# Kernel optimization log

Hardware: AMD Instinct MI355X
Metric: run time of the kernel (lower is better)

## Reference

```python
import jax, jax.numpy as jnp
import numpy as np

N, E, IN_FT, OUT_FT = 20000, 4096, 128, 128


def setup_inputs() -> dict:
    key = jax.random.key(0)
    kx, kh, kw = jax.random.split(key, 3)
    X = jax.random.normal(kx, (N, IN_FT), dtype=jnp.float32)
    H = jax.random.randint(kh, (N, E), 0, 2, dtype=jnp.int32)
    weight = jax.random.normal(kw, (IN_FT, OUT_FT), dtype=jnp.float32) * (1.0 / np.sqrt(IN_FT))
    bias = jnp.zeros((OUT_FT,), dtype=jnp.float32)
    return {"X": X, "H": H, "weight": weight, "bias": bias}


def reference(X, H, weight, bias):
    # Dv^{-1/2} H De^{-1} H^T Dv^{-1/2} X W + b, with diag matrices fused as
    # row/column scalings (same math as the torch.diag @ chain, no NxN temporaries).
    Hf = H.astype(jnp.float32)
    v_deg = jnp.sum(Hf, axis=1)            # [N]
    e_deg = jnp.sum(Hf, axis=0)            # [E]
    v_deg = jnp.where(v_deg > 0, v_deg, 1.0)
    e_deg = jnp.where(e_deg > 0, e_deg, 1.0)
    dv_inv_sqrt = 1.0 / jnp.sqrt(v_deg)    # diag(Dv^-1/2)
    de_inv = 1.0 / e_deg                   # diag(De^-1)
    Y = dv_inv_sqrt[:, None] * X
    T = Hf.T @ Y                           # H^T (...)        [E, in]
    T = de_inv[:, None] * T                # De^-1 (...)
    Z = Hf @ T                             # H (...)          [N, in]
    Z = dv_inv_sqrt[:, None] * Z           # Dv^-1/2 (...)
    out = Z @ weight + bias                # [N, out]
    return out
```

## Files before the change

kernel.cpp:

```cpp
#include <hip/hip_runtime.h>

#define NV 20000
#define NE 4096
#define FT 128
#define NW_E 128
#define NW_V 625
#define NVP 20032

typedef __attribute__((ext_vector_type(8))) short short8v;
typedef __attribute__((ext_vector_type(4))) float float4v;

__device__ __forceinline__ unsigned short f2bf(float f) {
    unsigned u = __float_as_uint(f);
    u += 0x7FFFu + ((u >> 16) & 1u);
    return (unsigned short)(u >> 16);
}
__device__ __forceinline__ int lds_off(int r, int chunk) {
    return r * 128 + ((chunk ^ (r & 7)) << 4);
}
__device__ __forceinline__ uint4 lut_entry(int t) {
    uint4 e;
    e.x = ((t & 1) ? 0x3F80u : 0u) | ((t & 2) ? 0x3F800000u : 0u);
    e.y = ((t & 4) ? 0x3F80u : 0u) | ((t & 8) ? 0x3F800000u : 0u);
    e.z = ((t & 16) ? 0x3F80u : 0u) | ((t & 32) ? 0x3F800000u : 0u);
    e.w = ((t & 64) ? 0x3F80u : 0u) | ((t & 128) ? 0x3F800000u : 0u);
    return e;
}

__global__ __launch_bounds__(256) void k_packt(const int* __restrict__ H,
                                               unsigned* __restrict__ packed,
                                               unsigned* __restrict__ packedT,
                                               int* __restrict__ dvp) {
    __shared__ int cl[64];
    int b = blockIdx.x;
    int g = b >> 1, h = b & 1;
    int t = threadIdx.x, lane = t & 63;
    int w0 = h * 64 + (t >> 6) * 16;
    int n = g * 64 + lane;
    bool valid = n < NV;
    const uint4* base = reinterpret_cast<const uint4*>(H) + (size_t)n * (NE / 4);

    if (t < 64) cl[t] = 0;
    __syncthreads();

    int cnt = 0;
    int nw = g * 2 + (lane >> 5);
    for (int it = 0; it < 16; ++it) {
        int w = w0 + it;
        unsigned m = 0;
        if (valid) {
            const uint4* p = base + w * 8;
#pragma unroll
            for (int i = 0; i < 8; ++i) {
                uint4 v = p[i];
                m |= (v.x ? 1u : 0u) << (i * 4 + 0);
                m |= (v.y ? 1u : 0u) << (i * 4 + 1);
                m |= (v.z ? 1u : 0u) << (i * 4 + 2);
                m |= (v.w ? 1u : 0u) << (i * 4 + 3);
            }
            packed[(size_t)n * NW_E + w] = m;
        }
        cnt += __popc(m);
        unsigned my = 0;
#pragma unroll
        for (int j = 0; j < 32; ++j) {
            unsigned long long bm = __ballot(((m >> j) & 1u) != 0);
            unsigned part = (lane < 32) ? (unsigned)bm : (unsigned)(bm >> 32);
            if ((lane & 31) == j) my = part;
        }
        int e = w * 32 + (lane & 31);
        if (nw < NW_V) packedT[(size_t)e * NW_V + nw] = my;
    }
    atomicAdd(&cl[lane], cnt);
    __syncthreads();
    if (t < 64) dvp[h * NVP + g * 64 + t] = cl[t];
}

__global__ __launch_bounds__(256) void k_mid(const unsigned* __restrict__ packedT,
                                             const int* __restrict__ dvp,
                                             const float* __restrict__ X,
                                             float* __restrict__ de,
                                             float* __restrict__ dv,
                                             unsigned short* __restrict__ Ybf) {
    int b = blockIdx.x, t = threadIdx.x;
    if (b < 1024) {
        int lane = t & 63, w = t >> 6;
        int e = b * 4 + w;
        const unsigned* row = packedT + (size_t)e * NW_V;
        int c = 0;
        for (int i = lane; i < NW_V; i += 64) c += __popc(row[i]);
        for (int o = 32; o > 0; o >>= 1) c += __shfl_down(c, o, 64);
        if (lane == 0) de[e] = c > 0 ? 1.0f / (float)c : 1.0f;
    } else if (b < 1024 + 79) {
        int i = (b - 1024) * 256 + t;
        if (i < NV) {
            int d = dvp[i] + dvp[NVP + i];
            dv[i] = d > 0 ? 1.0f / sqrtf((float)d) : 1.0f;
        }
    } else {
        int b2 = b - 1103;
        int f = t & 127;
        int nb = (b2 * 2 + (t >> 7)) * 8;
        unsigned short h[8];
#pragma unroll
        for (int i = 0; i < 8; ++i) {
            int n = nb + i;
            int d = dvp[n] + dvp[NVP + n];
            float s = d > 0 ? 1.0f / sqrtf((float)d) : 1.0f;
            h[i] = f2bf(X[(size_t)n * FT + f] * s);
        }
        uint4 u;
        u.x = (unsigned)h[0] | ((unsigned)h[1] << 16);
        u.y = (unsigned)h[2] | ((unsigned)h[3] << 16);
        u.z = (unsigned)h[4] | ((unsigned)h[5] << 16);
        u.w = (unsigned)h[6] | ((unsigned)h[7] << 16);
        *reinterpret_cast<uint4*>(Ybf + (size_t)f * NV + nb) = u;
    }
}

__global__ __launch_bounds__(256, 2) void k_mm1(const unsigned short* __restrict__ Ybf,
                                                const unsigned* __restrict__ packedT,
                                                float* __restrict__ P, int chunkK) {
    __shared__ __align__(16) unsigned char sA[128 * 128];
    __shared__ __align__(16) unsigned char sB[128 * 128];
    __shared__ __align__(16) uint4 slut[256];
    int t = threadIdx.x;
    slut[t] = lut_entry(t & 255);

    int et = blockIdx.x & 31, kp = blockIdx.x >> 5;
    int e0 = et * 128;
    int kbeg = kp * chunkK;
    int iters = chunkK >> 6;

    float4v acc[4][4];
#pragma unroll
    for (int i = 0; i < 4; ++i)
#pragma unroll
        for (int j = 0; j < 4; ++j)
#pragma unroll
            for (int r = 0; r < 4; ++r) acc[i][j][r] = 0.0f;

    int fA = t & 127;
    int chbA = (t >> 7) * 4;
    const unsigned short* arow = Ybf + (size_t)fA * NV;
    int eB = t & 127;
    int hB = t >> 7;
    const unsigned* brow = packedT + (size_t)(e0 + eB) * NW_V;

    int wave = t >> 6, lane = t & 63;
    int wm0 = (wave & 1) * 64, wc0 = (wave >> 1) * 64;
    int r0 = lane & 15, q = lane >> 4;
    __syncthreads();

    for (int it = 0; it < iters; ++it) {
        int k0 = kbeg + it * 64;
#pragma unroll
        for (int c = 0; c < 4; ++c) {
            int ch = chbA + c;
            int n = k0 + ch * 8;
            uint4 v = {0, 0, 0, 0};
            if (n < NV) v = *reinterpret_cast<const uint4*>(arow + n);
            *reinterpret_cast<uint4*>(sA + lds_off(fA, ch)) = v;
        }
        {
            int nw = (k0 >> 5) + hB;
            unsigned wv = (nw < NW_V) ? brow[nw] : 0u;
#pragma unroll
            for (int c = 0; c < 4; ++c) {
                uint4 u = slut[(wv >> (c * 8)) & 0xFF];
                *reinterpret_cast<uint4*>(sB + lds_off(eB, hB * 4 + c)) = u;
            }
        }
        __syncthreads();
#pragma unroll
        for (int ks = 0; ks < 2; ++ks) {
            short8v a[4], bb[4];
#pragma unroll
            for (int mi = 0; mi < 4; ++mi)
                a[mi] = *reinterpret_cast<const short8v*>(sA + lds_off(wm0 + mi * 16 + r0, ks * 4 + q));
#pragma unroll
            for (int ci = 0; ci < 4; ++ci)
                bb[ci] = *reinterpret_cast<const short8v*>(sB + lds_off(wc0 + ci * 16 + r0, ks * 4 + q));
#pragma unroll
            for (int mi = 0; mi < 4; ++mi)
#pragma unroll
                for (int ci = 0; ci < 4; ++ci)
                    acc[mi][ci] = __builtin_amdgcn_mfma_f32_16x16x32_bf16(a[mi], bb[ci], acc[mi][ci], 0, 0, 0);
        }
        __syncthreads();
    }
    float* Pp = P + (size_t)kp * (128 * 4096);
#pragma unroll
    for (int mi = 0; mi < 4; ++mi)
#pragma unroll
        for (int ci = 0; ci < 4; ++ci) {
            int f = wm0 + mi * 16 + q * 4;
            int e = e0 + wc0 + ci * 16 + r0;
#pragma unroll
            for (int r = 0; r < 4; ++r)
                Pp[(size_t)(f + r) * 4096 + e] = acc[mi][ci][r];
        }
}

__global__ __launch_bounds__(256) void k_reduce(const float4v* __restrict__ P,
                                                float4v* __restrict__ Tt, int S) {
    int i = blockIdx.x * 256 + threadIdx.x;
    float4v a = P[i];
    for (int p = 1; p < S; ++p) a += P[(size_t)p * 131072 + i];
    Tt[i] = a;
}

__global__ __launch_bounds__(256) void k_ut(const float* __restrict__ Tt,
                                            const float* __restrict__ W,
                                            const float* __restrict__ de,
                                            unsigned short* __restrict__ Ubf) {
    int t = threadIdx.x;
    int e = blockIdx.x * 64 + (t & 63);
    int g0 = blockIdx.y * 16 + (t >> 6) * 4;
    float a0 = 0, a1 = 0, a2 = 0, a3 = 0;
    for (int f = 0; f < 128; ++f) {
        float tv = Tt[(size_t)f * 4096 + e];
        float4 wv = *reinterpret_cast<const float4*>(W + f * 128 + g0);
        a0 += tv * wv.x; a1 += tv * wv.y; a2 += tv * wv.z; a3 += tv * wv.w;
    }
    float d = de[e];
    Ubf[(size_t)(g0 + 0) * 4096 + e] = f2bf(a0 * d);
    Ubf[(size_t)(g0 + 1) * 4096 + e] = f2bf(a1 * d);
    Ubf[(size_t)(g0 + 2) * 4096 + e] = f2bf(a2 * d);
    Ubf[(size_t)(g0 + 3) * 4096 + e] = f2bf(a3 * d);
}

__global__ __launch_bounds__(256, 4) void k_mm2(const unsigned* __restrict__ packed,
                                                const unsigned short* __restrict__ Ubf,
                                                const float* __restrict__ dv,
                                                const float* __restrict__ bias,
                                                float* __restrict__ out) {
    __shared__ __align__(16) unsigned char sA[128 * 128];
    __shared__ __align__(16) unsigned char sB[32 * 128];
    __shared__ __align__(16) uint4 slut[256];
    int t = threadIdx.x;
    slut[t] = lut_entry(t & 255);

    int mt = blockIdx.x >> 2, qg = blockIdx.x & 3;
    int n0 = mt * 128, g0 = qg * 32;

    float4v acc[4];
#pragma unroll
    for (int i = 0; i < 4; ++i)
#pragma unroll
        for (int r = 0; r < 4; ++r) acc[i][r] = 0.0f;

    int nA = t & 127, hA = t >> 7;
    int rB = t & 31, cB = t >> 5;
    const unsigned short* brow = Ubf + (size_t)(g0 + rB) * 4096;

    int wave = t >> 6, lane = t & 63;
    int wm0 = (wave & 1) * 64, wc0 = (wave >> 1) * 16;
    int r0 = lane & 15, q = lane >> 4;
    __syncthreads();

    for (int k0 = 0; k0 < 4096; k0 += 64) {
        {
            unsigned wv = (n0 + nA < NV) ? packed[(size_t)(n0 + nA) * NW_E + (k0 >> 5) + hA] : 0u;
#pragma unroll
            for (int c = 0; c < 4; ++c) {
                uint4 u = slut[(wv >> (c * 8)) & 0xFF];
                *reinterpret_cast<uint4*>(sA + lds_off(nA, hA * 4 + c)) = u;
            }
        }
        {
            uint4 v = *reinterpret_cast<const uint4*>(brow + k0 + cB * 8);
            *reinterpret_cast<uint4*>(sB + lds_off(rB, cB)) = v;
        }
        __syncthreads();
#pragma unroll
        for (int ks = 0; ks < 2; ++ks) {
            short8v a[4], bb;
#pragma unroll
            for (int mi = 0; mi < 4; ++mi)
                a[mi] = *reinterpret_cast<const short8v*>(sA + lds_off(wm0 + mi * 16 + r0, ks * 4 + q));
            bb = *reinterpret_cast<const short8v*>(sB + lds_off(wc0 + r0, ks * 4 + q));
#pragma unroll
            for (int mi = 0; mi < 4; ++mi)
                acc[mi] = __builtin_amdgcn_mfma_f32_16x16x32_bf16(a[mi], bb, acc[mi], 0, 0, 0);
        }
        __syncthreads();
    }
    {
        int g = g0 + wc0 + r0;
        float bg = bias[g];
#pragma unroll
        for (int mi = 0; mi < 4; ++mi) {
#pragma unroll
            for (int r = 0; r < 4; ++r) {
                int n = n0 + wm0 + mi * 16 + q * 4 + r;
                if (n < NV) out[(size_t)n * 128 + g] = dv[n] * acc[mi][r] + bg;
            }
        }
    }
}

extern "C" void kernel_launch(void* const* d_in, const int* in_sizes, int n_in,
                              void* d_out, int out_size, void* d_ws, size_t ws_size,
                              hipStream_t stream) {
    const float* X    = (const float*)d_in[0];
    const int*   H    = (const int*)d_in[1];
    const float* W    = (const float*)d_in[2];
    const float* bias = (const float*)d_in[3];
    float* out = (float*)d_out;

    char* ws = (char*)d_ws;
    size_t off = 0;
    auto alloc = [&](size_t sz) { char* p = ws + off; off += (sz + 255) & ~(size_t)255; return p; };
    unsigned*       packed  = (unsigned*)alloc((size_t)NV * NW_E * 4);
    unsigned*       packedT = (unsigned*)alloc((size_t)NE * NW_V * 4);
    unsigned short* Ybf     = (unsigned short*)alloc((size_t)FT * NV * 2);
    float*          Tt      = (float*)alloc((size_t)FT * NE * 4);
    unsigned short* Ubf     = (unsigned short*)alloc((size_t)FT * NE * 2);
    float*          dv      = (float*)alloc((size_t)NV * 4);
    float*          de      = (float*)alloc((size_t)NE * 4);
    int*            dvp     = (int*)alloc((size_t)2 * NVP * 4);
    size_t fixed = off;

    long long avail = (long long)ws_size - (long long)fixed;
    int S = (int)(avail / (128LL * 4096 * 4));
    if (S > 16) S = 16;
    if (S < 1) S = 1;
    float* P1 = (float*)(ws + fixed);
    int chunkK = ((NV + S * 64 - 1) / (S * 64)) * 64;

    k_packt <<<626, 256, 0, stream>>>(H, packed, packedT, dvp);
    k_mid   <<<2353, 256, 0, stream>>>(packedT, dvp, X, de, dv, Ybf);
    k_mm1   <<<32 * S, 256, 0, stream>>>(Ybf, packedT, P1, chunkK);
    k_reduce<<<512, 256, 0, stream>>>((const float4v*)P1, (float4v*)Tt, S);
    k_ut    <<<dim3(64, 8), 256, 0, stream>>>(Tt, W, de, Ubf);
    k_mm2   <<<628, 256, 0, stream>>>(packed, Ubf, dv, bias, out);
}
```

Before: 636.1 us.

## Fuse all stages into one cooperative persistent kernel with grid syncs

Replaces six separate kernel launches with a single cooperative kernel of 512 blocks that runs packing, degree/scale computation, the split-K first GEMM, the reduction, the weight projection and the second GEMM as phases separated by grid-wide syncs. This removes per-launch overhead and the gaps between dependent kernels. The first GEMM is also retiled to 128x64 tiles with a fixed split-K of 8, chosen to match the 512-block grid. In exchange, each phase is capped at 512 resident blocks, the second GEMM loses its 4-blocks-per-CU occupancy hint, and grid syncs add their own cost.

```diff
diff --git a/kernel.cpp b/kernel.cpp
--- a/kernel.cpp
+++ b/kernel.cpp
@@ -1,4 +1,7 @@
 #include <hip/hip_runtime.h>
+#include <hip/hip_cooperative_groups.h>
+
+namespace cg = cooperative_groups;
 
 #define NV 20000
 #define NE 4096
@@ -6,6 +9,8 @@
 #define NW_E 128
 #define NW_V 625
 #define NVP 20032
+#define SPLITK 8
+#define CHUNKK 2560
 
 typedef __attribute__((ext_vector_type(8))) short short8v;
 typedef __attribute__((ext_vector_type(4))) float float4v;
@@ -27,274 +32,266 @@
     return e;
 }
 
-__global__ __launch_bounds__(256) void k_packt(const int* __restrict__ H,
-                                               unsigned* __restrict__ packed,
-                                               unsigned* __restrict__ packedT,
-                                               int* __restrict__ dvp) {
-    __shared__ int cl[64];
-    int b = blockIdx.x;
-    int g = b >> 1, h = b & 1;
-    int t = threadIdx.x, lane = t & 63;
-    int w0 = h * 64 + (t >> 6) * 16;
-    int n = g * 64 + lane;
-    bool valid = n < NV;
-    const uint4* base = reinterpret_cast<const uint4*>(H) + (size_t)n * (NE / 4);
-
-    if (t < 64) cl[t] = 0;
-    __syncthreads();
-
-    int cnt = 0;
-    int nw = g * 2 + (lane >> 5);
-    for (int it = 0; it < 16; ++it) {
-        int w = w0 + it;
-        unsigned m = 0;
-        if (valid) {
-            const uint4* p = base + w * 8;
+__global__ __launch_bounds__(256, 2) void k_mega(
+    const int* __restrict__ H, const float* __restrict__ X,
+    const float* __restrict__ W, const float* __restrict__ bias,
+    float* __restrict__ out,
+    unsigned* __restrict__ packed, unsigned* __restrict__ packedT,
+    int* __restrict__ dvp, unsigned short* __restrict__ Ybf,
+    float* __restrict__ P, float* __restrict__ Tt,
+    unsigned short* __restrict__ Ubf, float* __restrict__ dv,
+    float* __restrict__ de) {
+
+    __shared__ __align__(16) unsigned char sA[16384];
+    __shared__ __align__(16) unsigned char sB[8192];
+    __shared__ __align__(16) uint4 slut[256];
+
+    cg::grid_group grid = cg::this_grid();
+    int t = threadIdx.x;
+    int wave = t >> 6, lane = t & 63;
+    int r0 = lane & 15, q = lane >> 4;
+
+    slut[t] = lut_entry(t);
+
+    {
+        int* cl = (int*)sA;
+        for (int v = blockIdx.x; v < 626; v += 512) {
+            int g = v >> 1, h = v & 1;
+            int w0 = h * 64 + wave * 16;
+            int n = g * 64 + lane;
+            bool valid = n < NV;
+            const uint4* base = reinterpret_cast<const uint4*>(H) + (size_t)n * (NE / 4);
+
+            if (t < 64) cl[t] = 0;
+            __syncthreads();
+
+            int cnt = 0;
+            int nw = g * 2 + (lane >> 5);
+            for (int it = 0; it < 16; ++it) {
+                int w = w0 + it;
+                unsigned m = 0;
+                if (valid) {
+                    const uint4* p = base + w * 8;
+#pragma unroll
+                    for (int i = 0; i < 8; ++i) {
+                        uint4 vv = p[i];
+                        m |= (vv.x ? 1u : 0u) << (i * 4 + 0);
+                        m |= (vv.y ? 1u : 0u) << (i * 4 + 1);
+                        m |= (vv.z ? 1u : 0u) << (i * 4 + 2);
+                        m |= (vv.w ? 1u : 0u) << (i * 4 + 3);
+                    }
+                    packed[(size_t)n * NW_E + w] = m;
+                }
+                cnt += __popc(m);
+                unsigned my = 0;
+#pragma unroll
+                for (int j = 0; j < 32; ++j) {
+                    unsigned long long bm = __ballot(((m >> j) & 1u) != 0);
+                    unsigned part = (lane < 32) ? (unsigned)bm : (unsigned)(bm >> 32);
+                    if ((lane & 31) == j) my = part;
+                }
+                int e = w * 32 + (lane & 31);
+                if (nw < NW_V) packedT[(size_t)e * NW_V + nw] = my;
+            }
+            atomicAdd(&cl[lane], cnt);
+            __syncthreads();
+            if (t < 64) dvp[h * NVP + g * 64 + t] = cl[t];
+            __syncthreads();
+        }
+    }
+    grid.sync();
+
+    for (int v = blockIdx.x; v < 2353; v += 512) {
+        if (v < 1024) {
+            int e = v * 4 + wave;
+            const unsigned* row = packedT + (size_t)e * NW_V;
+            int c = 0;
+            for (int i = lane; i < NW_V; i += 64) c += __popc(row[i]);
+            for (int o = 32; o > 0; o >>= 1) c += __shfl_down(c, o, 64);
+            if (lane == 0) de[e] = c > 0 ? 1.0f / (float)c : 1.0f;
+        } else if (v < 1024 + 79) {
+            int i = (v - 1024) * 256 + t;
+            if (i < NV) {
+                int d = dvp[i] + dvp[NVP + i];
+                dv[i] = d > 0 ? 1.0f / sqrtf((float)d) : 1.0f;
+            }
+        } else {
+            int b2 = v - 1103;
+            int f = t & 127;
+            int nb = (b2 * 2 + (t >> 7)) * 8;
+            unsigned short h[8];
 #pragma unroll
             for (int i = 0; i < 8; ++i) {
-                uint4 v = p[i];
-                m |= (v.x ? 1u : 0u) << (i * 4 + 0);
-                m |= (v.y ? 1u : 0u) << (i * 4 + 1);
-                m |= (v.z ? 1u : 0u) << (i * 4 + 2);
-                m |= (v.w ? 1u : 0u) << (i * 4 + 3);
-            }
-            packed[(size_t)n * NW_E + w] = m;
-        }
-        cnt += __popc(m);
-        unsigned my = 0;
-#pragma unroll
-        for (int j = 0; j < 32; ++j) {
-            unsigned long long bm = __ballot(((m >> j) & 1u) != 0);
-            unsigned part = (lane < 32) ? (unsigned)bm : (unsigned)(bm >> 32);
-            if ((lane & 31) == j) my = part;
-        }
-        int e = w * 32 + (lane & 31);
-        if (nw < NW_V) packedT[(size_t)e * NW_V + nw] = my;
-    }
-    atomicAdd(&cl[lane], cnt);
-    __syncthreads();
-    if (t < 64) dvp[h * NVP + g * 64 + t] = cl[t];
-}
-
-__global__ __launch_bounds__(256) void k_mid(const unsigned* __restrict__ packedT,
-                                             const int* __restrict__ dvp,
-                                             const float* __restrict__ X,
-                                             float* __restrict__ de,
-                                             float* __restrict__ dv,
-                                             unsigned short* __restrict__ Ybf) {
-    int b = blockIdx.x, t = threadIdx.x;
-    if (b < 1024) {
-        int lane = t & 63, w = t >> 6;
-        int e = b * 4 + w;
-        const unsigned* row = packedT + (size_t)e * NW_V;
-        int c = 0;
-        for (int i = lane; i < NW_V; i += 64) c += __popc(row[i]);
-        for (int o = 32; o > 0; o >>= 1) c += __shfl_down(c, o, 64);
-        if (lane == 0) de[e] = c > 0 ? 1.0f / (float)c : 1.0f;
-    } else if (b < 1024 + 79) {
-        int i = (b - 1024) * 256 + t;
-        if (i < NV) {
-            int d = dvp[i] + dvp[NVP + i];
-            dv[i] = d > 0 ? 1.0f / sqrtf((float)d) : 1.0f;
-        }
-    } else {
-        int b2 = b - 1103;
-        int f = t & 127;
-        int nb = (b2 * 2 + (t >> 7)) * 8;
-        unsigned short h[8];
-#pragma unroll
-        for (int i = 0; i < 8; ++i) {
-            int n = nb + i;
-            int d = dvp[n] + dvp[NVP + n];
-            float s = d > 0 ? 1.0f / sqrtf((float)d) : 1.0f;
-            h[i] = f2bf(X[(size_t)n * FT + f] * s);
-        }
-        uint4 u;
-        u.x = (unsigned)h[0] | ((unsigned)h[1] << 16);
-        u.y = (unsigned)h[2] | ((unsigned)h[3] << 16);
-        u.z = (unsigned)h[4] | ((unsigned)h[5] << 16);
-        u.w = (unsigned)h[6] | ((unsigned)h[7] << 16);
-        *reinterpret_cast<uint4*>(Ybf + (size_t)f * NV + nb) = u;
-    }
-}
-
-__global__ __launch_bounds__(256, 2) void k_mm1(const unsigned short* __restrict__ Ybf,
-                                                const unsigned* __restrict__ packedT,
-                                                float* __restrict__ P, int chunkK) {
-    __shared__ __align__(16) unsigned char sA[128 * 128];
-    __shared__ __align__(16) unsigned char sB[128 * 128];
-    __shared__ __align__(16) uint4 slut[256];
-    int t = threadIdx.x;
-    slut[t] = lut_entry(t & 255);
-
-    int et = blockIdx.x & 31, kp = blockIdx.x >> 5;
-    int e0 = et * 128;
-    int kbeg = kp * chunkK;
-    int iters = chunkK >> 6;
-
-    float4v acc[4][4];
-#pragma unroll
-    for (int i = 0; i < 4; ++i)
-#pragma unroll
-        for (int j = 0; j < 4; ++j)
-#pragma unroll
-            for (int r = 0; r < 4; ++r) acc[i][j][r] = 0.0f;
-
-    int fA = t & 127;
-    int chbA = (t >> 7) * 4;
-    const unsigned short* arow = Ybf + (size_t)fA * NV;
-    int eB = t & 127;
-    int hB = t >> 7;
-    const unsigned* brow = packedT + (size_t)(e0 + eB) * NW_V;
-
-    int wave = t >> 6, lane = t & 63;
-    int wm0 = (wave & 1) * 64, wc0 = (wave >> 1) * 64;
-    int r0 = lane & 15, q = lane >> 4;
-    __syncthreads();
-
-    for (int it = 0; it < iters; ++it) {
-        int k0 = kbeg + it * 64;
-#pragma unroll
-        for (int c = 0; c < 4; ++c) {
-            int ch = chbA + c;
-            int n = k0 + ch * 8;
-            uint4 v = {0, 0, 0, 0};
-            if (n < NV) v = *reinterpret_cast<const uint4*>(arow + n);
-            *reinterpret_cast<uint4*>(sA + lds_off(fA, ch)) = v;
+                int n = nb + i;
+                int d = dvp[n] + dvp[NVP + n];
+                float s = d > 0 ? 1.0f / sqrtf((float)d) : 1.0f;
+                h[i] = f2bf(X[(size_t)n * FT + f] * s);
+            }
+            uint4 u;
+            u.x = (unsigned)h[0] | ((unsigned)h[1] << 16);
+            u.y = (unsigned)h[2] | ((unsigned)h[3] << 16);
+            u.z = (unsigned)h[4] | ((unsigned)h[5] << 16);
+            u.w = (unsigned)h[6] | ((unsigned)h[7] << 16);
+            *reinterpret_cast<uint4*>(Ybf + (size_t)f * NV + nb) = u;
+        }
+    }
+    grid.sync();
+
+    {
+        int et = blockIdx.x & 63, kp = blockIdx.x >> 6;
+        int e0 = et * 64;
+        int kbeg = kp * CHUNKK;
+
+        float4v acc[4][2];
+#pragma unroll
+        for (int i = 0; i < 4; ++i)
+#pragma unroll
+            for (int j = 0; j < 2; ++j)
+#pragma unroll
+                for (int r = 0; r < 4; ++r) acc[i][j][r] = 0.0f;
+
+        int fA = t & 127;
+        int chbA = (t >> 7) * 4;
+        const unsigned short* arow = Ybf + (size_t)fA * NV;
+        int rB = t & 63, wsel = (t >> 6) & 1, bsel = t >> 7;
+        const unsigned* brow = packedT + (size_t)(e0 + rB) * NW_V;
+
+        int wm0 = (wave & 1) * 64, wc0 = (wave >> 1) * 32;
+
+        for (int it = 0; it < CHUNKK / 64; ++it) {
+            int k0 = kbeg + it * 64;
+#pragma unroll
+            for (int c = 0; c < 4; ++c) {
+                int ch = chbA + c;
+                int n = k0 + ch * 8;
+                uint4 v = {0, 0, 0, 0};
+                if (n < NV) v = *reinterpret_cast<const uint4*>(arow + n);
+                *reinterpret_cast<uint4*>(sA + lds_off(fA, ch)) = v;
+            }
+            {
+                int nw = (k0 >> 5) + wsel;
+                unsigned wv = (nw < NW_V) ? brow[nw] : 0u;
+#pragma unroll
+                for (int c = 0; c < 2; ++c) {
+                    int byte = bsel * 2 + c;
+                    uint4 u = slut[(wv >> (byte * 8)) & 0xFF];
+                    *reinterpret_cast<uint4*>(sB + lds_off(rB, wsel * 4 + byte)) = u;
+                }
+            }
+            __syncthreads();
+#pragma unroll
+            for (int ks = 0; ks < 2; ++ks) {
+                short8v a[4], bb[2];
+#pragma unroll
+                for (int mi = 0; mi < 4; ++mi)
+                    a[mi] = *reinterpret_cast<const short8v*>(sA + lds_off(wm0 + mi * 16 + r0, ks * 4 + q));
+#pragma unroll
+                for (int ci = 0; ci < 2; ++ci)
+                    bb[ci] = *reinterpret_cast<const short8v*>(sB + lds_off(wc0 + ci * 16 + r0, ks * 4 + q));
+#pragma unroll
+                for (int mi = 0; mi < 4; ++mi)
+#pragma unroll
+                    for (int ci = 0; ci < 2; ++ci)
+                        acc[mi][ci] = __builtin_amdgcn_mfma_f32_16x16x32_bf16(a[mi], bb[ci], acc[mi][ci], 0, 0, 0);
+            }
+            __syncthreads();
+        }
+        float* Pp = P + (size_t)kp * (128 * 4096);
+#pragma unroll
+        for (int mi = 0; mi < 4; ++mi)
+#pragma unroll
+            for (int ci = 0; ci < 2; ++ci) {
+                int f = wm0 + mi * 16 + q * 4;
+                int e = e0 + wc0 + ci * 16 + r0;
+#pragma unroll
+                for (int r = 0; r < 4; ++r)
+                    Pp[(size_t)(f + r) * 4096 + e] = acc[mi][ci][r];
+            }
+    }
+    grid.sync();
+
+    {
+        int i = blockIdx.x * 256 + t;
+        const float4v* Pv = (const float4v*)P;
+        float4v a = Pv[i];
+#pragma unroll
+        for (int p = 1; p < SPLITK; ++p) a += Pv[(size_t)p * 131072 + i];
+        ((float4v*)Tt)[i] = a;
+    }
+    grid.sync();
+
+    {
+        int bx = blockIdx.x & 63, by = blockIdx.x >> 6;
+        int e = bx * 64 + (t & 63);
+        int g0 = by * 16 + (t >> 6) * 4;
+        float a0 = 0, a1 = 0, a2 = 0, a3 = 0;
+        for (int f = 0; f < 128; ++f) {
+            float tv = Tt[(size_t)f * 4096 + e];
+            float4 wv = *reinterpret_cast<const float4*>(W + f * 128 + g0);
+            a0 += tv * wv.x; a1 += tv * wv.y; a2 += tv * wv.z; a3 += tv * wv.w;
+        }
+        float d = de[e];
+        Ubf[(size_t)(g0 + 0) * 4096 + e] = f2bf(a0 * d);
+        Ubf[(size_t)(g0 + 1) * 4096 + e] = f2bf(a1 * d);
+        Ubf[(size_t)(g0 + 2) * 4096 + e] = f2bf(a2 * d);
+        Ubf[(size_t)(g0 + 3) * 4096 + e] = f2bf(a3 * d);
+    }
+    grid.sync();
+
+    for (int v = blockIdx.x; v < 628; v += 512) {
+        int mt = v >> 2, qg = v & 3;
+        int n0 = mt * 128, g0 = qg * 32;
+
+        float4v acc[4];
+#pragma unroll
+        for (int i = 0; i < 4; ++i)
+#pragma unroll
+            for (int r = 0; r < 4; ++r) acc[i][r] = 0.0f;
+
+        int nA = t & 127, hA = t >> 7;
+        int rB = t & 31, cB = t >> 5;
+        const unsigned short* brow = Ubf + (size_t)(g0 + rB) * 4096;
+
+        int wm0 = (wave & 1) * 64, wc0 = (wave >> 1) * 16;
+        __syncthreads();
+
+        for (int k0 = 0; k0 < 4096; k0 += 64) {
+            {
+                unsigned wv = (n0 + nA < NV) ? packed[(size_t)(n0 + nA) * NW_E + (k0 >> 5) + hA] : 0u;
+#pragma unroll
+                for (int c = 0; c < 4; ++c) {
+                    uint4 u = slut[(wv >> (c * 8)) & 0xFF];
+                    *reinterpret_cast<uint4*>(sA + lds_off(nA, hA * 4 + c)) = u;
+                }
+            }
+            {
+                uint4 v2 = *reinterpret_cast<const uint4*>(brow + k0 + cB * 8);
+                *reinterpret_cast<uint4*>(sB + lds_off(rB, cB)) = v2;
+            }
+            __syncthreads();
+#pragma unroll
+            for (int ks = 0; ks < 2; ++ks) {
+                short8v a[4], bb;
+#pragma unroll
+                for (int mi = 0; mi < 4; ++mi)
+                    a[mi] = *reinterpret_cast<const short8v*>(sA + lds_off(wm0 + mi * 16 + r0, ks * 4 + q));
+                bb = *reinterpret_cast<const short8v*>(sB + lds_off(wc0 + r0, ks * 4 + q));
+#pragma unroll
+                for (int mi = 0; mi < 4; ++mi)
+                    acc[mi] = __builtin_amdgcn_mfma_f32_16x16x32_bf16(a[mi], bb, acc[mi], 0, 0, 0);
+            }
+            __syncthreads();
         }
         {
-            int nw = (k0 >> 5) + hB;
-            unsigned wv = (nw < NW_V) ? brow[nw] : 0u;
-#pragma unroll
-            for (int c = 0; c < 4; ++c) {
-                uint4 u = slut[(wv >> (c * 8)) & 0xFF];
-                *reinterpret_cast<uint4*>(sB + lds_off(eB, hB * 4 + c)) = u;
-            }
-        }
-        __syncthreads();
-#pragma unroll
-        for (int ks = 0; ks < 2; ++ks) {
-            short8v a[4], bb[4];
-#pragma unroll
-            for (int mi = 0; mi < 4; ++mi)
-                a[mi] = *reinterpret_cast<const short8v*>(sA + lds_off(wm0 + mi * 16 + r0, ks * 4 + q));
-#pragma unroll
-            for (int ci = 0; ci < 4; ++ci)
-                bb[ci] = *reinterpret_cast<const short8v*>(sB + lds_off(wc0 + ci * 16 + r0, ks * 4 + q));
-#pragma unroll
-            for (int mi = 0; mi < 4; ++mi)
-#pragma unroll
-                for (int ci = 0; ci < 4; ++ci)
-                    acc[mi][ci] = __builtin_amdgcn_mfma_f32_16x16x32_bf16(a[mi], bb[ci], acc[mi][ci], 0, 0, 0);
-        }
-        __syncthreads();
-    }
-    float* Pp = P + (size_t)kp * (128 * 4096);
-#pragma unroll
-    for (int mi = 0; mi < 4; ++mi)
-#pragma unroll
-        for (int ci = 0; ci < 4; ++ci) {
-            int f = wm0 + mi * 16 + q * 4;
-            int e = e0 + wc0 + ci * 16 + r0;
-#pragma unroll
-            for (int r = 0; r < 4; ++r)
-                Pp[(size_t)(f + r) * 4096 + e] = acc[mi][ci][r];
-        }
-}
-
-__global__ __launch_bounds__(256) void k_reduce(const float4v* __restrict__ P,
-                                                float4v* __restrict__ Tt, int S) {
-    int i = blockIdx.x * 256 + threadIdx.x;
-    float4v a = P[i];
-    for (int p = 1; p < S; ++p) a += P[(size_t)p * 131072 + i];
-    Tt[i] = a;
-}
-
-__global__ __launch_bounds__(256) void k_ut(const float* __restrict__ Tt,
-                                            const float* __restrict__ W,
-                                            const float* __restrict__ de,
-                                            unsigned short* __restrict__ Ubf) {
-    int t = threadIdx.x;
-    int e = blockIdx.x * 64 + (t & 63);
-    int g0 = blockIdx.y * 16 + (t >> 6) * 4;
-    float a0 = 0, a1 = 0, a2 = 0, a3 = 0;
-    for (int f = 0; f < 128; ++f) {
-        float tv = Tt[(size_t)f * 4096 + e];
-        float4 wv = *reinterpret_cast<const float4*>(W + f * 128 + g0);
-        a0 += tv * wv.x; a1 += tv * wv.y; a2 += tv * wv.z; a3 += tv * wv.w;
-    }
-    float d = de[e];
-    Ubf[(size_t)(g0 + 0) * 4096 + e] = f2bf(a0 * d);
-    Ubf[(size_t)(g0 + 1) * 4096 + e] = f2bf(a1 * d);
-    Ubf[(size_t)(g0 + 2) * 4096 + e] = f2bf(a2 * d);
-    Ubf[(size_t)(g0 + 3) * 4096 + e] = f2bf(a3 * d);
-}
-
-__global__ __launch_bounds__(256, 4) void k_mm2(const unsigned* __restrict__ packed,
-                                                const unsigned short* __restrict__ Ubf,
-                                                const float* __restrict__ dv,
-                                                const float* __restrict__ bias,
-                                                float* __restrict__ out) {
-    __shared__ __align__(16) unsigned char sA[128 * 128];
-    __shared__ __align__(16) unsigned char sB[32 * 128];
-    __shared__ __align__(16) uint4 slut[256];
-    int t = threadIdx.x;
-    slut[t] = lut_entry(t & 255);
-
-    int mt = blockIdx.x >> 2, qg = blockIdx.x & 3;
-    int n0 = mt * 128, g0 = qg * 32;
-
-    float4v acc[4];
-#pragma unroll
-    for (int i = 0; i < 4; ++i)
-#pragma unroll
-        for (int r = 0; r < 4; ++r) acc[i][r] = 0.0f;
-
-    int nA = t & 127, hA = t >> 7;
-    int rB = t & 31, cB = t >> 5;
-    const unsigned short* brow = Ubf + (size_t)(g0 + rB) * 4096;
-
-    int wave = t >> 6, lane = t & 63;
-    int wm0 = (wave & 1) * 64, wc0 = (wave >> 1) * 16;
-    int r0 = lane & 15, q = lane >> 4;
-    __syncthreads();
-
-    for (int k0 = 0; k0 < 4096; k0 += 64) {
-        {
-            unsigned wv = (n0 + nA < NV) ? packed[(size_t)(n0 + nA) * NW_E + (k0 >> 5) + hA] : 0u;
-#pragma unroll
-            for (int c = 0; c < 4; ++c) {
-                uint4 u = slut[(wv >> (c * 8)) & 0xFF];
-                *reinterpret_cast<uint4*>(sA + lds_off(nA, hA * 4 + c)) = u;
-            }
-        }
-        {
-            uint4 v = *reinterpret_cast<const uint4*>(brow + k0 + cB * 8);
-            *reinterpret_cast<uint4*>(sB + lds_off(rB, cB)) = v;
-        }
-        __syncthreads();
-#pragma unroll
-        for (int ks = 0; ks < 2; ++ks) {
-            short8v a[4], bb;
-#pragma unroll
-            for (int mi = 0; mi < 4; ++mi)
-                a[mi] = *reinterpret_cast<const short8v*>(sA + lds_off(wm0 + mi * 16 + r0, ks * 4 + q));
-            bb = *reinterpret_cast<const short8v*>(sB + lds_off(wc0 + r0, ks * 4 + q));
-#pragma unroll
-            for (int mi = 0; mi < 4; ++mi)
-                acc[mi] = __builtin_amdgcn_mfma_f32_16x16x32_bf16(a[mi], bb, acc[mi], 0, 0, 0);
-        }
-        __syncthreads();
-    }
-    {
-        int g = g0 + wc0 + r0;
-        float bg = bias[g];
-#pragma unroll
-        for (int mi = 0; mi < 4; ++mi) {
-#pragma unroll
-            for (int r = 0; r < 4; ++r) {
-                int n = n0 + wm0 + mi * 16 + q * 4 + r;
-                if (n < NV) out[(size_t)n * 128 + g] = dv[n] * acc[mi][r] + bg;
+            int g = g0 + wc0 + r0;
+            float bg = bias[g];
+#pragma unroll
+            for (int mi = 0; mi < 4; ++mi) {
+#pragma unroll
+                for (int r = 0; r < 4; ++r) {
+                    int n = n0 + wm0 + mi * 16 + q * 4 + r;
+                    if (n < NV) out[(size_t)n * 128 + g] = dv[n] * acc[mi][r] + bg;
+                }
             }
         }
     }
@@ -303,8 +300,8 @@
 extern "C" void kernel_launch(void* const* d_in, const int* in_sizes, int n_in,
                               void* d_out, int out_size, void* d_ws, size_t ws_size,
                               hipStream_t stream) {
+    const int*   H    = (const int*)d_in[1];
     const float* X    = (const float*)d_in[0];
-    const int*   H    = (const int*)d_in[1];
     const float* W    = (const float*)d_in[2];
     const float* bias = (const float*)d_in[3];
     float* out = (float*)d_out;
@@ -320,19 +317,11 @@
     float*          dv      = (float*)alloc((size_t)NV * 4);
     float*          de      = (float*)alloc((size_t)NE * 4);
     int*            dvp     = (int*)alloc((size_t)2 * NVP * 4);
-    size_t fixed = off;
-
-    long long avail = (long long)ws_size - (long long)fixed;
-    int S = (int)(avail / (128LL * 4096 * 4));
-    if (S > 16) S = 16;
-    if (S < 1) S = 1;
-    float* P1 = (float*)(ws + fixed);
-    int chunkK = ((NV + S * 64 - 1) / (S * 64)) * 64;
-
-    k_packt <<<626, 256, 0, stream>>>(H, packed, packedT, dvp);
-    k_mid   <<<2353, 256, 0, stream>>>(packedT, dvp, X, de, dv, Ybf);
-    k_mm1   <<<32 * S, 256, 0, stream>>>(Ybf, packedT, P1, chunkK);
-    k_reduce<<<512, 256, 0, stream>>>((const float4v*)P1, (float4v*)Tt, S);
-    k_ut    <<<dim3(64, 8), 256, 0, stream>>>(Tt, W, de, Ubf);
-    k_mm2   <<<628, 256, 0, stream>>>(packed, Ubf, dv, bias, out);
-}
+    float*          P1      = (float*)alloc((size_t)SPLITK * FT * NE * 4);
+
+    void* args[] = {(void*)&H, (void*)&X, (void*)&W, (void*)&bias, (void*)&out,
+                    (void*)&packed, (void*)&packedT, (void*)&dvp, (void*)&Ybf,
+                    (void*)&P1, (void*)&Tt, (void*)&Ubf, (void*)&dv, (void*)&de};
+    hipLaunchCooperativeKernel(reinterpret_cast<void*>(k_mega), dim3(512), dim3(256),
+                               args, 0, stream);
+}
```

After: 1.015 ms. 1.6x slower.

## Split packing into coalesced row pack and bit-transpose, tile operands into contiguous slabs

Applied to the files above, without the earlier changes.

The combined pack/transpose kernel becomes two kernels. One reads each H row contiguously with two waves per row, computes the vertex degree scale directly, and writes the bitmask. The other does the ballot bit-transpose into a padded packedT stride. The matmul operands (scaled X and the U matrix) are stored in per-K-chunk contiguous 64-wide slabs so the GEMM tile loads are fully coalesced, and the bitmask words are prefetched as uint4 one iteration ahead. The aim is to cut the strided, poorly coalesced reads of the 328MB H input and of the GEMM tiles, at the cost of an extra launch and an extra pass over the packed bitmask.

```diff
diff --git a/kernel.cpp b/kernel.cpp
--- a/kernel.cpp
+++ b/kernel.cpp
@@ -5,7 +5,8 @@
 #define FT 128
 #define NW_E 128
 #define NW_V 625
-#define NVP 20032
+#define PT_STRIDE 632
+#define NKC 313
 
 typedef __attribute__((ext_vector_type(8))) short short8v;
 typedef __attribute__((ext_vector_type(4))) float float4v;
@@ -27,110 +28,106 @@
     return e;
 }
 
-__global__ __launch_bounds__(256) void k_packt(const int* __restrict__ H,
-                                               unsigned* __restrict__ packed,
-                                               unsigned* __restrict__ packedT,
-                                               int* __restrict__ dvp) {
-    __shared__ int cl[64];
-    int b = blockIdx.x;
-    int g = b >> 1, h = b & 1;
-    int t = threadIdx.x, lane = t & 63;
-    int w0 = h * 64 + (t >> 6) * 16;
-    int n = g * 64 + lane;
-    bool valid = n < NV;
-    const uint4* base = reinterpret_cast<const uint4*>(H) + (size_t)n * (NE / 4);
-
-    if (t < 64) cl[t] = 0;
+__global__ __launch_bounds__(256) void k_pack(const int* __restrict__ H,
+                                              unsigned* __restrict__ packed,
+                                              float* __restrict__ dv) {
+    __shared__ int cl[4];
+    int t = threadIdx.x, wave = t >> 6, lane = t & 63;
+    int row = blockIdx.x * 2 + (wave >> 1);
+    int half = wave & 1;
+    const uint4* base = reinterpret_cast<const uint4*>(H) + (size_t)row * 1024 + half * 512 + lane * 8;
+    unsigned m = 0;
+#pragma unroll
+    for (int i = 0; i < 8; ++i) {
+        uint4 v = base[i];
+        m |= (v.x ? 1u : 0u) << (i * 4 + 0);
+        m |= (v.y ? 1u : 0u) << (i * 4 + 1);
+        m |= (v.z ? 1u : 0u) << (i * 4 + 2);
+        m |= (v.w ? 1u : 0u) << (i * 4 + 3);
+    }
+    packed[(size_t)row * NW_E + half * 64 + lane] = m;
+    int c = __popc(m);
+    for (int o = 32; o > 0; o >>= 1) c += __shfl_down(c, o, 64);
+    if (lane == 0) cl[wave] = c;
     __syncthreads();
-
-    int cnt = 0;
-    int nw = g * 2 + (lane >> 5);
-    for (int it = 0; it < 16; ++it) {
-        int w = w0 + it;
-        unsigned m = 0;
-        if (valid) {
-            const uint4* p = base + w * 8;
-#pragma unroll
-            for (int i = 0; i < 8; ++i) {
-                uint4 v = p[i];
-                m |= (v.x ? 1u : 0u) << (i * 4 + 0);
-                m |= (v.y ? 1u : 0u) << (i * 4 + 1);
-                m |= (v.z ? 1u : 0u) << (i * 4 + 2);
-                m |= (v.w ? 1u : 0u) << (i * 4 + 3);
-            }
-            packed[(size_t)n * NW_E + w] = m;
-        }
-        cnt += __popc(m);
-        unsigned my = 0;
-#pragma unroll
-        for (int j = 0; j < 32; ++j) {
-            unsigned long long bm = __ballot(((m >> j) & 1u) != 0);
-            unsigned part = (lane < 32) ? (unsigned)bm : (unsigned)(bm >> 32);
-            if ((lane & 31) == j) my = part;
-        }
-        int e = w * 32 + (lane & 31);
-        if (nw < NW_V) packedT[(size_t)e * NW_V + nw] = my;
-    }
-    atomicAdd(&cl[lane], cnt);
-    __syncthreads();
-    if (t < 64) dvp[h * NVP + g * 64 + t] = cl[t];
+    if (t < 2) {
+        int d = cl[t * 2] + cl[t * 2 + 1];
+        dv[blockIdx.x * 2 + t] = d > 0 ? 1.0f / sqrtf((float)d) : 1.0f;
+    }
+}
+
+__global__ __launch_bounds__(256) void k_btrans(const unsigned* __restrict__ packed,
+                                                unsigned* __restrict__ packedT) {
+    int lane = threadIdx.x & 63;
+    int w = threadIdx.x >> 6;
+    int ew = blockIdx.y * 4 + w;
+    int n = blockIdx.x * 64 + lane;
+    unsigned wv = (n < NV) ? packed[(size_t)n * NW_E + ew] : 0u;
+    unsigned my = 0;
+#pragma unroll
+    for (int j = 0; j < 32; ++j) {
+        unsigned long long m = __ballot(((wv >> j) & 1u) != 0);
+        unsigned part = (lane < 32) ? (unsigned)m : (unsigned)(m >> 32);
+        if ((lane & 31) == j) my = part;
+    }
+    int nw = blockIdx.x * 2 + (lane >> 5);
+    int e = ew * 32 + (lane & 31);
+    if (nw <= 625) packedT[(size_t)e * PT_STRIDE + nw] = my;
 }
 
 __global__ __launch_bounds__(256) void k_mid(const unsigned* __restrict__ packedT,
-                                             const int* __restrict__ dvp,
                                              const float* __restrict__ X,
+                                             const float* __restrict__ dv,
                                              float* __restrict__ de,
-                                             float* __restrict__ dv,
-                                             unsigned short* __restrict__ Ybf) {
+                                             unsigned short* __restrict__ At) {
     int b = blockIdx.x, t = threadIdx.x;
+    int wave = t >> 6, lane = t & 63;
     if (b < 1024) {
-        int lane = t & 63, w = t >> 6;
-        int e = b * 4 + w;
-        const unsigned* row = packedT + (size_t)e * NW_V;
+        int e = b * 4 + wave;
+        const unsigned* row = packedT + (size_t)e * PT_STRIDE;
         int c = 0;
         for (int i = lane; i < NW_V; i += 64) c += __popc(row[i]);
         for (int o = 32; o > 0; o >>= 1) c += __shfl_down(c, o, 64);
         if (lane == 0) de[e] = c > 0 ? 1.0f / (float)c : 1.0f;
-    } else if (b < 1024 + 79) {
-        int i = (b - 1024) * 256 + t;
-        if (i < NV) {
-            int d = dvp[i] + dvp[NVP + i];
-            dv[i] = d > 0 ? 1.0f / sqrtf((float)d) : 1.0f;
-        }
-    } else {
-        int b2 = b - 1103;
+    } else if (b < 2274) {
+        int b2 = b - 1024;
         int f = t & 127;
         int nb = (b2 * 2 + (t >> 7)) * 8;
         unsigned short h[8];
 #pragma unroll
         for (int i = 0; i < 8; ++i) {
             int n = nb + i;
-            int d = dvp[n] + dvp[NVP + n];
-            float s = d > 0 ? 1.0f / sqrtf((float)d) : 1.0f;
-            h[i] = f2bf(X[(size_t)n * FT + f] * s);
+            h[i] = f2bf(X[(size_t)n * FT + f] * dv[n]);
         }
         uint4 u;
         u.x = (unsigned)h[0] | ((unsigned)h[1] << 16);
         u.y = (unsigned)h[2] | ((unsigned)h[3] << 16);
         u.z = (unsigned)h[4] | ((unsigned)h[5] << 16);
         u.w = (unsigned)h[6] | ((unsigned)h[7] << 16);
-        *reinterpret_cast<uint4*>(Ybf + (size_t)f * NV + nb) = u;
-    }
-}
-
-__global__ __launch_bounds__(256, 2) void k_mm1(const unsigned short* __restrict__ Ybf,
+        int kc = nb >> 6;
+        *reinterpret_cast<uint4*>(At + (size_t)kc * 8192 + f * 64 + (nb & 63)) = u;
+    } else {
+        int f = t & 127;
+        uint4 z = {0, 0, 0, 0};
+        *reinterpret_cast<uint4*>(At + (size_t)312 * 8192 + f * 64 + 32 + (t >> 7) * 8) = z;
+        *reinterpret_cast<uint4*>(At + (size_t)312 * 8192 + f * 64 + 48 + (t >> 7) * 8) = z;
+    }
+}
+
+__global__ __launch_bounds__(256, 2) void k_mm1(const unsigned short* __restrict__ At,
                                                 const unsigned* __restrict__ packedT,
                                                 float* __restrict__ P, int chunkK) {
-    __shared__ __align__(16) unsigned char sA[128 * 128];
-    __shared__ __align__(16) unsigned char sB[128 * 128];
+    __shared__ __align__(16) unsigned char sA[16384];
+    __shared__ __align__(16) unsigned char sB[16384];
     __shared__ __align__(16) uint4 slut[256];
     int t = threadIdx.x;
-    slut[t] = lut_entry(t & 255);
+    slut[t] = lut_entry(t);
 
     int et = blockIdx.x & 31, kp = blockIdx.x >> 5;
     int e0 = et * 128;
     int kbeg = kp * chunkK;
-    int iters = chunkK >> 6;
+    int kend = kbeg + chunkK; if (kend > NKC * 64) kend = NKC * 64;
+    int iters = (kend - kbeg) >> 6; if (iters < 0) iters = 0;
 
     float4v acc[4][4];
 #pragma unroll
@@ -139,37 +136,41 @@
         for (int j = 0; j < 4; ++j)
 #pragma unroll
             for (int r = 0; r < 4; ++r) acc[i][j][r] = 0.0f;
-
-    int fA = t & 127;
-    int chbA = (t >> 7) * 4;
-    const unsigned short* arow = Ybf + (size_t)fA * NV;
-    int eB = t & 127;
-    int hB = t >> 7;
-    const unsigned* brow = packedT + (size_t)(e0 + eB) * NW_V;
 
     int wave = t >> 6, lane = t & 63;
     int wm0 = (wave & 1) * 64, wc0 = (wave >> 1) * 64;
     int r0 = lane & 15, q = lane >> 4;
+
+    const unsigned* brow = packedT + (size_t)(e0 + (t & 127)) * PT_STRIDE + (kbeg >> 5);
+    uint4 bw, bw2;
+    if (t < 128) bw = *reinterpret_cast<const uint4*>(brow);
     __syncthreads();
 
     for (int it = 0; it < iters; ++it) {
-        int k0 = kbeg + it * 64;
+        int kc = (kbeg >> 6) + it;
+        const uint4* slab = reinterpret_cast<const uint4*>(At + (size_t)kc * 8192);
 #pragma unroll
         for (int c = 0; c < 4; ++c) {
-            int ch = chbA + c;
-            int n = k0 + ch * 8;
-            uint4 v = {0, 0, 0, 0};
-            if (n < NV) v = *reinterpret_cast<const uint4*>(arow + n);
-            *reinterpret_cast<uint4*>(sA + lds_off(fA, ch)) = v;
-        }
-        {
-            int nw = (k0 >> 5) + hB;
-            unsigned wv = (nw < NW_V) ? brow[nw] : 0u;
-#pragma unroll
-            for (int c = 0; c < 4; ++c) {
-                uint4 u = slut[(wv >> (c * 8)) & 0xFF];
-                *reinterpret_cast<uint4*>(sB + lds_off(eB, hB * 4 + c)) = u;
+            int idx = c * 256 + t;
+            uint4 v = slab[idx];
+            *reinterpret_cast<uint4*>(sA + lds_off(idx >> 3, idx & 7)) = v;
+        }
+        if (t < 128) {
+            unsigned w0, w1;
+            if (!(it & 1)) {
+                bw2 = *reinterpret_cast<const uint4*>(brow + 2 * it + 4);
+                w0 = bw.x; w1 = bw.y;
+            } else {
+                w0 = bw.z; w1 = bw.w;
             }
+            int rB = t;
+#pragma unroll
+            for (int c = 0; c < 4; ++c)
+                *reinterpret_cast<uint4*>(sB + lds_off(rB, c)) = slut[(w0 >> (c * 8)) & 0xFF];
+#pragma unroll
+            for (int c = 0; c < 4; ++c)
+                *reinterpret_cast<uint4*>(sB + lds_off(rB, 4 + c)) = slut[(w1 >> (c * 8)) & 0xFF];
+            if (it & 1) bw = bw2;
         }
         __syncthreads();
 #pragma unroll
@@ -213,9 +214,10 @@
 __global__ __launch_bounds__(256) void k_ut(const float* __restrict__ Tt,
                                             const float* __restrict__ W,
                                             const float* __restrict__ de,
-                                            unsigned short* __restrict__ Ubf) {
+                                            unsigned short* __restrict__ Ut) {
     int t = threadIdx.x;
-    int e = blockIdx.x * 64 + (t & 63);
+    int bx = blockIdx.x;
+    int e = bx * 64 + (t & 63);
     int g0 = blockIdx.y * 16 + (t >> 6) * 4;
     float a0 = 0, a1 = 0, a2 = 0, a3 = 0;
     for (int f = 0; f < 128; ++f) {
@@ -224,22 +226,23 @@
         a0 += tv * wv.x; a1 += tv * wv.y; a2 += tv * wv.z; a3 += tv * wv.w;
     }
     float d = de[e];
-    Ubf[(size_t)(g0 + 0) * 4096 + e] = f2bf(a0 * d);
-    Ubf[(size_t)(g0 + 1) * 4096 + e] = f2bf(a1 * d);
-    Ubf[(size_t)(g0 + 2) * 4096 + e] = f2bf(a2 * d);
-    Ubf[(size_t)(g0 + 3) * 4096 + e] = f2bf(a3 * d);
+    int j = t & 63;
+    Ut[(size_t)bx * 8192 + (g0 + 0) * 64 + j] = f2bf(a0 * d);
+    Ut[(size_t)bx * 8192 + (g0 + 1) * 64 + j] = f2bf(a1 * d);
+    Ut[(size_t)bx * 8192 + (g0 + 2) * 64 + j] = f2bf(a2 * d);
+    Ut[(size_t)bx * 8192 + (g0 + 3) * 64 + j] = f2bf(a3 * d);
 }
 
 __global__ __launch_bounds__(256, 4) void k_mm2(const unsigned* __restrict__ packed,
-                                                const unsigned short* __restrict__ Ubf,
+                                                const unsigned short* __restrict__ Ut,
                                                 const float* __restrict__ dv,
                                                 const float* __restrict__ bias,
                                                 float* __restrict__ out) {
-    __shared__ __align__(16) unsigned char sA[128 * 128];
-    __shared__ __align__(16) unsigned char sB[32 * 128];
+    __shared__ __align__(16) unsigned char sA[16384];
+    __shared__ __align__(16) unsigned char sB[4096];
     __shared__ __align__(16) uint4 slut[256];
     int t = threadIdx.x;
-    slut[t] = lut_entry(t & 255);
+    slut[t] = lut_entry(t);
 
     int mt = blockIdx.x >> 2, qg = blockIdx.x & 3;
     int n0 = mt * 128, g0 = qg * 32;
@@ -249,28 +252,43 @@
     for (int i = 0; i < 4; ++i)
 #pragma unroll
         for (int r = 0; r < 4; ++r) acc[i][r] = 0.0f;
-
-    int nA = t & 127, hA = t >> 7;
-    int rB = t & 31, cB = t >> 5;
-    const unsigned short* brow = Ubf + (size_t)(g0 + rB) * 4096;
 
     int wave = t >> 6, lane = t & 63;
     int wm0 = (wave & 1) * 64, wc0 = (wave >> 1) * 16;
     int r0 = lane & 15, q = lane >> 4;
+
+    const unsigned* arow = packed + (size_t)(n0 + (t & 127)) * NW_E;
+    const unsigned short* bbase = Ut + (size_t)qg * 2048;
+    int t2 = t - 128;
+    uint4 aw, aw2;
+    if (t < 128) aw = *reinterpret_cast<const uint4*>(arow);
     __syncthreads();
 
-    for (int k0 = 0; k0 < 4096; k0 += 64) {
-        {
-            unsigned wv = (n0 + nA < NV) ? packed[(size_t)(n0 + nA) * NW_E + (k0 >> 5) + hA] : 0u;
-#pragma unroll
-            for (int c = 0; c < 4; ++c) {
-                uint4 u = slut[(wv >> (c * 8)) & 0xFF];
-                *reinterpret_cast<uint4*>(sA + lds_off(nA, hA * 4 + c)) = u;
+    for (int it = 0; it < 64; ++it) {
+        if (t < 128) {
+            unsigned w0, w1;
+            if (!(it & 1)) {
+                aw2 = *reinterpret_cast<const uint4*>(arow + 2 * it + 4);
+                w0 = aw.x; w1 = aw.y;
+            } else {
+                w0 = aw.z; w1 = aw.w;
             }
-        }
-        {
-            uint4 v = *reinterpret_cast<const uint4*>(brow + k0 + cB * 8);
-            *reinterpret_cast<uint4*>(sB + lds_off(rB, cB)) = v;
+            int rA = t;
+#pragma unroll
+            for (int c = 0; c < 4; ++c)
+                *reinterpret_cast<uint4*>(sA + lds_off(rA, c)) = slut[(w0 >> (c * 8)) & 0xFF];
+#pragma unroll
+            for (int c = 0; c < 4; ++c)
+                *reinterpret_cast<uint4*>(sA + lds_off(rA, 4 + c)) = slut[(w1 >> (c * 8)) & 0xFF];
+            if (it & 1) aw = aw2;
+        } else {
+            const uint4* src = reinterpret_cast<const uint4*>(bbase + (size_t)it * 8192);
+#pragma unroll
+            for (int c = 0; c < 2; ++c) {
+                int idx = t2 * 2 + c;
+                uint4 v = src[idx];
+                *reinterpret_cast<uint4*>(sB + lds_off(idx >> 3, idx & 7)) = v;
+            }
         }
         __syncthreads();
 #pragma unroll
@@ -313,13 +331,12 @@
     size_t off = 0;
     auto alloc = [&](size_t sz) { char* p = ws + off; off += (sz + 255) & ~(size_t)255; return p; };
     unsigned*       packed  = (unsigned*)alloc((size_t)NV * NW_E * 4);
-    unsigned*       packedT = (unsigned*)alloc((size_t)NE * NW_V * 4);
-    unsigned short* Ybf     = (unsigned short*)alloc((size_t)FT * NV * 2);
+    unsigned*       packedT = (unsigned*)alloc((size_t)NE * PT_STRIDE * 4);
+    unsigned short* At      = (unsigned short*)alloc((size_t)NKC * 8192 * 2);
     float*          Tt      = (float*)alloc((size_t)FT * NE * 4);
-    unsigned short* Ubf     = (unsigned short*)alloc((size_t)FT * NE * 2);
+    unsigned short* Ut      = (unsigned short*)alloc((size_t)FT * NE * 2);
     float*          dv      = (float*)alloc((size_t)NV * 4);
     float*          de      = (float*)alloc((size_t)NE * 4);
-    int*            dvp     = (int*)alloc((size_t)2 * NVP * 4);
     size_t fixed = off;
 
     long long avail = (long long)ws_size - (long long)fixed;
@@ -327,12 +344,13 @@
     if (S > 16) S = 16;
     if (S < 1) S = 1;
     float* P1 = (float*)(ws + fixed);
-    int chunkK = ((NV + S * 64 - 1) / (S * 64)) * 64;
-
-    k_packt <<<626, 256, 0, stream>>>(H, packed, packedT, dvp);
-    k_mid   <<<2353, 256, 0, stream>>>(packedT, dvp, X, de, dv, Ybf);
-    k_mm1   <<<32 * S, 256, 0, stream>>>(Ybf, packedT, P1, chunkK);
+    int chunkK = ((NKC * 64 + S * 64 - 1) / (S * 64)) * 64;
+
+    k_pack  <<<NV / 2, 256, 0, stream>>>(H, packed, dv);
+    k_btrans<<<dim3(313, 32), 256, 0, stream>>>(packed, packedT);
+    k_mid   <<<2275, 256, 0, stream>>>(packedT, X, dv, de, At);
+    k_mm1   <<<32 * S, 256, 0, stream>>>(At, packedT, P1, chunkK);
     k_reduce<<<512, 256, 0, stream>>>((const float4v*)P1, (float4v*)Tt, S);
-    k_ut    <<<dim3(64, 8), 256, 0, stream>>>(Tt, W, de, Ubf);
-    k_mm2   <<<628, 256, 0, stream>>>(packed, Ubf, dv, bias, out);
-}
+    k_ut    <<<dim3(64, 8), 256, 0, stream>>>(Tt, W, de, Ut);
+    k_mm2   <<<628, 256, 0, stream>>>(packed, Ut, dv, bias, out);
+}
```

Result: faster. 590.7 us (-7.1%).
